# Kernel optimization log

Hardware: AMD Instinct MI355X
Metric: run time of the kernel (lower is better)

The kernel has to match this reference:

```python
import jax, jax.numpy as jnp
import numpy as np

TOKEN_DIM = 1024
N_HEADS = 16
HEAD_DIM = TOKEN_DIM // N_HEADS  # 64
B, S = 8, 1024


def setup_inputs() -> dict:
    key = jax.random.key(0)
    ks = jax.random.split(key, 7)
    scale = 1.0 / np.sqrt(HEAD_DIM)
    token_seq = jax.random.normal(ks[0], (B, S, TOKEN_DIM), dtype=jnp.float32)
    Wq = jax.random.normal(ks[1], (N_HEADS, HEAD_DIM, HEAD_DIM), dtype=jnp.float32) * scale
    Wk = jax.random.normal(ks[2], (N_HEADS, HEAD_DIM, HEAD_DIM), dtype=jnp.float32) * scale
    Wv = jax.random.normal(ks[3], (N_HEADS, HEAD_DIM, HEAD_DIM), dtype=jnp.float32) * scale
    bq = jax.random.normal(ks[4], (N_HEADS, HEAD_DIM), dtype=jnp.float32) * 0.01
    bk = jax.random.normal(ks[5], (N_HEADS, HEAD_DIM), dtype=jnp.float32) * 0.01
    bv = jax.random.normal(ks[6], (N_HEADS, HEAD_DIM), dtype=jnp.float32) * 0.01
    return {"token_seq": token_seq, "Wq": Wq, "Wk": Wk, "Wv": Wv,
            "bq": bq, "bk": bk, "bv": bv}


def reference(token_seq, Wq, Wk, Wv, bq, bk, bv):
    b, s, d = token_seq.shape
    x = token_seq.reshape(b, s, N_HEADS, HEAD_DIM)  # [B,S,H,hd]
    # Per-head linear projections (torch nn.Linear per head, batched as einsum)
    q = jnp.einsum('bshd,hde->bshe', x, Wq) + bq  # [B,S,H,hd]
    k = jnp.einsum('bshd,hde->bshe', x, Wk) + bk
    v = jnp.einsum('bshd,hde->bshe', x, Wv) + bv
    inv_sqrt_d = jnp.asarray(1.0 / np.sqrt(HEAD_DIM), dtype=token_seq.dtype)
    scores = jnp.einsum('bshe,bthe->bhst', q, k) * inv_sqrt_d  # [B,H,S,S]
    attn = jax.nn.softmax(scores, axis=-1)
    out = jnp.einsum('bhst,bthe->bshe', attn, v)  # [B,S,H,hd]
    # concat over heads along last dim == reshape
    return out.reshape(b, s, d)
```

## Files before the change

kernel.cpp:

```cpp
#include <hip/hip_runtime.h>
#include <stdint.h>

#define NH 16
#define HD 64
#define BB 8
#define SS 1024
#define TD 1024

typedef _Float16 f16;
typedef __attribute__((ext_vector_type(8))) f16 f16x8;
typedef __attribute__((ext_vector_type(16))) float f32x16;

#define MFMA32(a, b, c) __builtin_amdgcn_mfma_f32_32x32x16_f16((a), (b), (c), 0, 0, 0)
#define SW(r, c) (((r) << 7) + ((c) ^ (((r) & 7) << 4)))

__device__ __forceinline__ unsigned pkrtz(float a, float b) {
    auto r = __builtin_amdgcn_cvt_pkrtz(a, b);
    return __builtin_bit_cast(unsigned, r);
}
__device__ __forceinline__ unsigned h16(float a) {
    f16 h = (f16)a;
    return (unsigned)__builtin_bit_cast(unsigned short, h);
}
__device__ __forceinline__ unsigned pk_rtne(float a, float b) {
    return h16(a) | (h16(b) << 16);
}
__device__ __forceinline__ void gload16(const void* g, void* l) {
    __builtin_amdgcn_global_load_lds(
        (const __attribute__((address_space(1))) unsigned int*)g,
        (__attribute__((address_space(3))) unsigned int*)l, 16, 0, 0);
}

__global__ __launch_bounds__(256) void proj_kernel(
    const float* __restrict__ x,
    const float* __restrict__ Wq, const float* __restrict__ Wk, const float* __restrict__ Wv,
    const float* __restrict__ bq, const float* __restrict__ bk, const float* __restrict__ bv,
    f16* __restrict__ qo, f16* __restrict__ ko, f16* __restrict__ vo)
{
    __shared__ __align__(16) char lds[40960];
    const int stile = blockIdx.x, h = blockIdx.y, b = blockIdx.z;
    const int t = threadIdx.x;
    const int s0 = stile * 128;
    const int pair = b * NH + h;

    {
        const int row = t >> 1, half = t & 1;
        const float* src = x + ((size_t)b * SS + s0 + row) * TD + h * HD + half * 32;
        #pragma unroll
        for (int i = 0; i < 8; ++i) {
            float4 v4 = *(const float4*)(src + i * 4);
            const int cb = half * 64 + i * 8;
            *(unsigned*)(lds + SW(row, cb))     = pk_rtne(v4.x, v4.y);
            *(unsigned*)(lds + SW(row, cb + 4)) = pk_rtne(v4.z, v4.w);
        }
    }
    {
        const int e = t & 63, dg = t >> 6;
        const float* Ws[3] = {Wq, Wk, Wv};
        #pragma unroll
        for (int z = 0; z < 3; ++z) {
            const float* src = Ws[z] + (size_t)h * 4096 + (size_t)dg * 16 * 64 + e;
            char* base = lds + 16384 + z * 8192;
            #pragma unroll
            for (int j = 0; j < 8; ++j) {
                const float a0 = src[(2 * j) * 64], a1 = src[(2 * j + 1) * 64];
                const int cb = dg * 32 + j * 4;
                *(unsigned*)(base + SW(e, cb)) = pk_rtne(a0, a1);
            }
        }
    }
    __syncthreads();

    const int w = t >> 6, l = t & 63, l31 = l & 31, hi = l >> 5;
    const float* bs[3] = {bq, bk, bv};

    f16x8 xa[4];
    #pragma unroll
    for (int c = 0; c < 4; ++c)
        xa[c] = *(const f16x8*)(lds + SW(w * 32 + l31, c * 32 + hi * 16));

    #pragma unroll
    for (int z = 0; z < 2; ++z) {
        const char* wb = lds + 16384 + z * 8192;
        f32x16 acc[2] = {};
        #pragma unroll
        for (int nt = 0; nt < 2; ++nt)
            #pragma unroll
            for (int c = 0; c < 4; ++c) {
                f16x8 wf = *(const f16x8*)(wb + SW(nt * 32 + l31, c * 32 + hi * 16));
                acc[nt] = MFMA32(xa[c], wf, acc[nt]);
            }
        const float scl = (z == 0) ? 0.125f * 1.44269504088896f : 1.0f;
        f16* dst = (z == 0) ? qo : ko;
        #pragma unroll
        for (int nt = 0; nt < 2; ++nt) {
            const int e = nt * 32 + l31;
            const float bb = bs[z][h * 64 + e];
            #pragma unroll
            for (int r = 0; r < 16; ++r) {
                const int sl = w * 32 + (r & 3) + 8 * (r >> 2) + 4 * hi;
                dst[(size_t)pair * 65536 + (size_t)(s0 + sl) * 64 + e] =
                    (f16)((acc[nt][r] + bb) * scl);
            }
        }
    }
    {
        const char* wb = lds + 16384 + 2 * 8192;
        const int mt = w & 1, ng = w >> 1;
        f16x8 wv[4];
        #pragma unroll
        for (int c = 0; c < 4; ++c)
            wv[c] = *(const f16x8*)(wb + SW(mt * 32 + l31, c * 32 + hi * 16));
        float bvv[16];
        #pragma unroll
        for (int r = 0; r < 16; ++r)
            bvv[r] = bs[2][h * 64 + mt * 32 + (r & 3) + 8 * (r >> 2) + 4 * hi];
        f32x16 acc[2] = {};
        #pragma unroll
        for (int j = 0; j < 2; ++j) {
            const int srow = (ng * 2 + j) * 32 + l31;
            #pragma unroll
            for (int c = 0; c < 4; ++c) {
                f16x8 xf = *(const f16x8*)(lds + SW(srow, c * 32 + hi * 16));
                acc[j] = MFMA32(wv[c], xf, acc[j]);
            }
        }
        #pragma unroll
        for (int j = 0; j < 2; ++j) {
            const int sl = (ng * 2 + j) * 32 + l31;
            #pragma unroll
            for (int r = 0; r < 16; ++r) {
                const int e = mt * 32 + (r & 3) + 8 * (r >> 2) + 4 * hi;
                vo[(size_t)pair * 65536 + (size_t)e * 1024 + s0 + sl] =
                    (f16)(acc[j][r] + bvv[r]);
            }
        }
    }
}

__global__ __launch_bounds__(256, 4) void attn_kernel(
    const f16* __restrict__ qf, const f16* __restrict__ kf,
    const f16* __restrict__ vt, float* __restrict__ out)
{
    __shared__ __align__(16) char lds[32768];

    const int p = blockIdx.x;
    const int id = (p & 7) * 128 + (p >> 3);
    const int st = id & 7;
    const int pr = id >> 3;
    const int h = pr & (NH - 1), b = pr >> 4;

    const int t = threadIdx.x, w = t >> 6, l = t & 63, l31 = l & 31, hi = l >> 5;

    f16x8 qfr[4];
    {
        const char* qp = (const char*)(qf + (size_t)pr * 65536)
                       + (size_t)(st * 128 + w * 32 + l31) * 128;
        #pragma unroll
        for (int c = 0; c < 4; ++c)
            qfr[c] = *(const f16x8*)(qp + c * 32 + hi * 16);
    }

    int koff[2], voff[2];
    #pragma unroll
    for (int j = 0; j < 2; ++j) {
        const int o = j * 4096 + w * 1024 + l * 16;
        const int r = o >> 7, c = o & 127;
        const int cs = c ^ ((r & 7) << 4);
        koff[j] = r * 128 + cs;
        voff[j] = r * 2048 + cs;
    }
    const char* kB = (const char*)(kf + (size_t)pr * 65536);
    const char* vB = (const char*)(vt + (size_t)pr * 65536);

    auto stage = [&](int kt, int base) {
        #pragma unroll
        for (int j = 0; j < 2; ++j) {
            char* ld = lds + base + j * 4096 + w * 1024;
            gload16(kB + (size_t)kt * 8192 + koff[j], ld);
            gload16(vB + (size_t)kt * 128 + voff[j], ld + 8192);
        }
    };

    float m = -3e38f, lsum = 0.f;
    f32x16 o_[2] = {};

    stage(0, 0);

    for (int kt = 0; kt < 16; ++kt) {
        __syncthreads();
        const int X = (kt & 1) ? 16384 : 0;
        if (kt < 15) stage(kt + 1, 16384 - X);

        f32x16 s_[2] = {};
        #pragma unroll
        for (int jt = 0; jt < 2; ++jt)
            #pragma unroll
            for (int c = 0; c < 4; ++c) {
                f16x8 kfr = *(const f16x8*)(lds + X + SW(jt * 32 + l31, c * 32 + hi * 16));
                s_[jt] = MFMA32(kfr, qfr[c], s_[jt]);
            }

        float mm = s_[0][0];
        #pragma unroll
        for (int i = 1; i < 16; ++i) mm = fmaxf(mm, s_[0][i]);
        #pragma unroll
        for (int i = 0; i < 16; ++i) mm = fmaxf(mm, s_[1][i]);
        mm = fmaxf(mm, __shfl_xor(mm, 32));
        const float nm = fmaxf(m, mm);
        const float sc = __builtin_amdgcn_exp2f(m - nm);
        m = nm;
        float ps = 0.f;
        #pragma unroll
        for (int jt = 0; jt < 2; ++jt)
            #pragma unroll
            for (int i = 0; i < 16; ++i) {
                const float e = __builtin_amdgcn_exp2f(s_[jt][i] - nm);
                s_[jt][i] = e;
                ps += e;
            }
        ps += __shfl_xor(ps, 32);
        lsum = lsum * sc + ps;
        #pragma unroll
        for (int i = 0; i < 16; ++i) { o_[0][i] *= sc; o_[1][i] *= sc; }

        #pragma unroll
        for (int jt = 0; jt < 2; ++jt) {
            unsigned u[8];
            #pragma unroll
            for (int a = 0; a < 4; ++a) {
                u[2 * a]     = pkrtz(s_[jt][4 * a],     s_[jt][4 * a + 1]);
                u[2 * a + 1] = pkrtz(s_[jt][4 * a + 2], s_[jt][4 * a + 3]);
            }
            {
                auto r0 = __builtin_amdgcn_permlane32_swap(u[0], u[2], false, false);
                u[0] = r0[0]; u[2] = r0[1];
                auto r1 = __builtin_amdgcn_permlane32_swap(u[1], u[3], false, false);
                u[1] = r1[0]; u[3] = r1[1];
                auto r2 = __builtin_amdgcn_permlane32_swap(u[4], u[6], false, false);
                u[4] = r2[0]; u[6] = r2[1];
                auto r3 = __builtin_amdgcn_permlane32_swap(u[5], u[7], false, false);
                u[5] = r3[0]; u[7] = r3[1];
            }
            #pragma unroll
            for (int cl = 0; cl < 2; ++cl) {
                uint4 pu = {u[cl * 4], u[cl * 4 + 1], u[cl * 4 + 2], u[cl * 4 + 3]};
                f16x8 pf = __builtin_bit_cast(f16x8, pu);
                const int cv = jt * 2 + cl;
                #pragma unroll
                for (int mt = 0; mt < 2; ++mt) {
                    f16x8 vf = *(const f16x8*)(lds + X + 8192 + SW(mt * 32 + l31, cv * 32 + hi * 16));
                    o_[mt] = MFMA32(vf, pf, o_[mt]);
                }
            }
        }
    }

    const float inv = 1.0f / lsum;
    const size_t row = (size_t)b * SS + st * 128 + w * 32 + l31;
    float* op = out + row * TD + h * 64;
    #pragma unroll
    for (int mt = 0; mt < 2; ++mt)
        #pragma unroll
        for (int g = 0; g < 4; ++g) {
            const int e0 = mt * 32 + 8 * g + 4 * hi;
            float4 o4 = {o_[mt][4 * g] * inv, o_[mt][4 * g + 1] * inv,
                         o_[mt][4 * g + 2] * inv, o_[mt][4 * g + 3] * inv};
            *(float4*)(op + e0) = o4;
        }
}

extern "C" void kernel_launch(void* const* d_in, const int* in_sizes, int n_in,
                              void* d_out, int out_size, void* d_ws, size_t ws_size,
                              hipStream_t stream) {
    const float* x  = (const float*)d_in[0];
    const float* Wq = (const float*)d_in[1];
    const float* Wk = (const float*)d_in[2];
    const float* Wv = (const float*)d_in[3];
    const float* bq = (const float*)d_in[4];
    const float* bk = (const float*)d_in[5];
    const float* bv = (const float*)d_in[6];
    float* outp = (float*)d_out;

    const size_t per = (size_t)BB * NH * SS * HD;
    f16* q  = (f16*)d_ws;
    f16* k  = q + per;
    f16* vt = k + per;

    proj_kernel<<<dim3(SS / 128, NH, BB), dim3(256), 0, stream>>>(
        x, Wq, Wk, Wv, bq, bk, bv, q, k, vt);
    attn_kernel<<<dim3(1024), dim3(256), 0, stream>>>(q, k, vt, outp);
}
```

Before: 147.9 us.

## Add lazy softmax rescaling, packed f16 row sums, and vectorized projection stores

In the attention kernel, the running max and the rescale of the accumulators are updated only when some lane's tile max exceeds the current max by more than 8 (in log2 units). This skips most per-tile exp and multiply work on the output accumulators. Row sums are now computed from the packed f16 probabilities with half-precision vector adds, the max uses a tree reduction, LDS addresses are precomputed, and the loop is unrolled by two. The projection kernel swaps MFMA operand order so each lane owns contiguous outputs, which allows packed 8-byte stores instead of scalar f16 stores. The risks are f16 rounding in the sums and a larger dynamic range in the unnormalized exponentials.

```diff
diff --git a/kernel.cpp b/kernel.cpp
--- a/kernel.cpp
+++ b/kernel.cpp
@@ -8,6 +8,7 @@
 #define TD 1024
 
 typedef _Float16 f16;
+typedef __attribute__((ext_vector_type(2))) f16 h2;
 typedef __attribute__((ext_vector_type(8))) f16 f16x8;
 typedef __attribute__((ext_vector_type(16))) float f32x16;
 
@@ -18,6 +19,7 @@
     auto r = __builtin_amdgcn_cvt_pkrtz(a, b);
     return __builtin_bit_cast(unsigned, r);
 }
+__device__ __forceinline__ h2 B2(unsigned u) { return __builtin_bit_cast(h2, u); }
 __device__ __forceinline__ unsigned h16(float a) {
     f16 h = (f16)a;
     return (unsigned)__builtin_bit_cast(unsigned short, h);
@@ -88,21 +90,24 @@
             #pragma unroll
             for (int c = 0; c < 4; ++c) {
                 f16x8 wf = *(const f16x8*)(wb + SW(nt * 32 + l31, c * 32 + hi * 16));
-                acc[nt] = MFMA32(xa[c], wf, acc[nt]);
+                acc[nt] = MFMA32(wf, xa[c], acc[nt]);
             }
         const float scl = (z == 0) ? 0.125f * 1.44269504088896f : 1.0f;
-        f16* dst = (z == 0) ? qo : ko;
-        #pragma unroll
-        for (int nt = 0; nt < 2; ++nt) {
-            const int e = nt * 32 + l31;
-            const float bb = bs[z][h * 64 + e];
-            #pragma unroll
-            for (int r = 0; r < 16; ++r) {
-                const int sl = w * 32 + (r & 3) + 8 * (r >> 2) + 4 * hi;
-                dst[(size_t)pair * 65536 + (size_t)(s0 + sl) * 64 + e] =
-                    (f16)((acc[nt][r] + bb) * scl);
-            }
-        }
+        f16* row_ptr = ((z == 0) ? qo : ko)
+                     + (size_t)pair * 65536 + (size_t)(s0 + w * 32 + l31) * 64;
+        #pragma unroll
+        for (int nt = 0; nt < 2; ++nt)
+            #pragma unroll
+            for (int g = 0; g < 4; ++g) {
+                const int e0 = nt * 32 + 8 * g + 4 * hi;
+                const float4 bb = *(const float4*)(bs[z] + h * 64 + e0);
+                const float v0 = (acc[nt][4 * g + 0] + bb.x) * scl;
+                const float v1 = (acc[nt][4 * g + 1] + bb.y) * scl;
+                const float v2 = (acc[nt][4 * g + 2] + bb.z) * scl;
+                const float v3 = (acc[nt][4 * g + 3] + bb.w) * scl;
+                uint2 pv = {pk_rtne(v0, v1), pk_rtne(v2, v3)};
+                *(uint2*)(row_ptr + e0) = pv;
+            }
     }
     {
         const char* wb = lds + 16384 + 2 * 8192;
@@ -111,28 +116,26 @@
         #pragma unroll
         for (int c = 0; c < 4; ++c)
             wv[c] = *(const f16x8*)(wb + SW(mt * 32 + l31, c * 32 + hi * 16));
-        float bvv[16];
-        #pragma unroll
-        for (int r = 0; r < 16; ++r)
-            bvv[r] = bs[2][h * 64 + mt * 32 + (r & 3) + 8 * (r >> 2) + 4 * hi];
-        f32x16 acc[2] = {};
+        const float bvv = bs[2][h * 64 + mt * 32 + l31];
+        f16* vrow = vo + (size_t)pair * 65536 + (size_t)(mt * 32 + l31) * 1024 + s0;
         #pragma unroll
         for (int j = 0; j < 2; ++j) {
-            const int srow = (ng * 2 + j) * 32 + l31;
+            const int srow = (ng * 2 + j) * 32;
+            f32x16 acc = {};
             #pragma unroll
             for (int c = 0; c < 4; ++c) {
-                f16x8 xf = *(const f16x8*)(lds + SW(srow, c * 32 + hi * 16));
-                acc[j] = MFMA32(wv[c], xf, acc[j]);
-            }
-        }
-        #pragma unroll
-        for (int j = 0; j < 2; ++j) {
-            const int sl = (ng * 2 + j) * 32 + l31;
-            #pragma unroll
-            for (int r = 0; r < 16; ++r) {
-                const int e = mt * 32 + (r & 3) + 8 * (r >> 2) + 4 * hi;
-                vo[(size_t)pair * 65536 + (size_t)e * 1024 + s0 + sl] =
-                    (f16)(acc[j][r] + bvv[r]);
+                f16x8 xf = *(const f16x8*)(lds + SW(srow + l31, c * 32 + hi * 16));
+                acc = MFMA32(xf, wv[c], acc);
+            }
+            #pragma unroll
+            for (int g = 0; g < 4; ++g) {
+                const int sb = srow + 8 * g + 4 * hi;
+                const float v0 = acc[4 * g + 0] + bvv;
+                const float v1 = acc[4 * g + 1] + bvv;
+                const float v2 = acc[4 * g + 2] + bvv;
+                const float v3 = acc[4 * g + 3] + bvv;
+                uint2 pv = {pk_rtne(v0, v1), pk_rtne(v2, v3)};
+                *(uint2*)(vrow + sb) = pv;
             }
         }
     }
@@ -160,6 +163,11 @@
         for (int c = 0; c < 4; ++c)
             qfr[c] = *(const f16x8*)(qp + c * 32 + hi * 16);
     }
+
+    int adr[4];
+    #pragma unroll
+    for (int c = 0; c < 4; ++c)
+        adr[c] = (l31 << 7) + ((c * 32 + hi * 16) ^ ((l31 & 7) << 4));
 
     int koff[2], voff[2];
     #pragma unroll
@@ -187,69 +195,86 @@
 
     stage(0, 0);
 
+    #pragma unroll 2
     for (int kt = 0; kt < 16; ++kt) {
         __syncthreads();
-        const int X = (kt & 1) ? 16384 : 0;
-        if (kt < 15) stage(kt + 1, 16384 - X);
+        const int X = (kt & 1) << 14;
+        if (kt < 15) stage(kt + 1, X ^ 16384);
 
         f32x16 s_[2] = {};
         #pragma unroll
         for (int jt = 0; jt < 2; ++jt)
             #pragma unroll
             for (int c = 0; c < 4; ++c) {
-                f16x8 kfr = *(const f16x8*)(lds + X + SW(jt * 32 + l31, c * 32 + hi * 16));
+                f16x8 kfr = *(const f16x8*)(lds + X + jt * 4096 + adr[c]);
                 s_[jt] = MFMA32(kfr, qfr[c], s_[jt]);
             }
 
-        float mm = s_[0][0];
-        #pragma unroll
-        for (int i = 1; i < 16; ++i) mm = fmaxf(mm, s_[0][i]);
-        #pragma unroll
-        for (int i = 0; i < 16; ++i) mm = fmaxf(mm, s_[1][i]);
-        mm = fmaxf(mm, __shfl_xor(mm, 32));
-        const float nm = fmaxf(m, mm);
-        const float sc = __builtin_amdgcn_exp2f(m - nm);
-        m = nm;
-        float ps = 0.f;
+        float red[16];
+        #pragma unroll
+        for (int i = 0; i < 16; ++i) red[i] = fmaxf(s_[0][i], s_[1][i]);
+        #pragma unroll
+        for (int off = 8; off >= 1; off >>= 1)
+            #pragma unroll
+            for (int i = 0; i < off; ++i) red[i] = fmaxf(red[i], red[i + off]);
+        float mx = fmaxf(red[0], __shfl_xor(red[0], 32));
+
+        if (__any(mx > m + 8.0f)) {
+            const float nm = fmaxf(m, mx);
+            const float sc = __builtin_amdgcn_exp2f(m - nm);
+            m = nm;
+            lsum *= sc;
+            #pragma unroll
+            for (int i = 0; i < 16; ++i) { o_[0][i] *= sc; o_[1][i] *= sc; }
+        }
+
         #pragma unroll
         for (int jt = 0; jt < 2; ++jt)
             #pragma unroll
-            for (int i = 0; i < 16; ++i) {
-                const float e = __builtin_amdgcn_exp2f(s_[jt][i] - nm);
-                s_[jt][i] = e;
-                ps += e;
-            }
-        ps += __shfl_xor(ps, 32);
-        lsum = lsum * sc + ps;
-        #pragma unroll
-        for (int i = 0; i < 16; ++i) { o_[0][i] *= sc; o_[1][i] *= sc; }
+            for (int i = 0; i < 16; ++i)
+                s_[jt][i] = __builtin_amdgcn_exp2f(s_[jt][i] - m);
+
+        unsigned u[2][8];
+        #pragma unroll
+        for (int jt = 0; jt < 2; ++jt)
+            #pragma unroll
+            for (int a = 0; a < 4; ++a) {
+                u[jt][2 * a]     = pkrtz(s_[jt][4 * a],     s_[jt][4 * a + 1]);
+                u[jt][2 * a + 1] = pkrtz(s_[jt][4 * a + 2], s_[jt][4 * a + 3]);
+            }
+
+        {
+            h2 t0 = (B2(u[0][0]) + B2(u[0][1])) + (B2(u[0][2]) + B2(u[0][3]));
+            h2 t1 = (B2(u[0][4]) + B2(u[0][5])) + (B2(u[0][6]) + B2(u[0][7]));
+            h2 t2 = (B2(u[1][0]) + B2(u[1][1])) + (B2(u[1][2]) + B2(u[1][3]));
+            h2 t3 = (B2(u[1][4]) + B2(u[1][5])) + (B2(u[1][6]) + B2(u[1][7]));
+            h2 tt = (t0 + t1) + (t2 + t3);
+            float ps = (float)tt[0] + (float)tt[1];
+            ps += __shfl_xor(ps, 32);
+            lsum += ps;
+        }
 
         #pragma unroll
         for (int jt = 0; jt < 2; ++jt) {
-            unsigned u[8];
-            #pragma unroll
-            for (int a = 0; a < 4; ++a) {
-                u[2 * a]     = pkrtz(s_[jt][4 * a],     s_[jt][4 * a + 1]);
-                u[2 * a + 1] = pkrtz(s_[jt][4 * a + 2], s_[jt][4 * a + 3]);
-            }
+            unsigned* uj = u[jt];
             {
-                auto r0 = __builtin_amdgcn_permlane32_swap(u[0], u[2], false, false);
-                u[0] = r0[0]; u[2] = r0[1];
-                auto r1 = __builtin_amdgcn_permlane32_swap(u[1], u[3], false, false);
-                u[1] = r1[0]; u[3] = r1[1];
-                auto r2 = __builtin_amdgcn_permlane32_swap(u[4], u[6], false, false);
-                u[4] = r2[0]; u[6] = r2[1];
-                auto r3 = __builtin_amdgcn_permlane32_swap(u[5], u[7], false, false);
-                u[5] = r3[0]; u[7] = r3[1];
+                auto r0 = __builtin_amdgcn_permlane32_swap(uj[0], uj[2], false, false);
+                uj[0] = r0[0]; uj[2] = r0[1];
+                auto r1 = __builtin_amdgcn_permlane32_swap(uj[1], uj[3], false, false);
+                uj[1] = r1[0]; uj[3] = r1[1];
+                auto r2 = __builtin_amdgcn_permlane32_swap(uj[4], uj[6], false, false);
+                uj[4] = r2[0]; uj[6] = r2[1];
+                auto r3 = __builtin_amdgcn_permlane32_swap(uj[5], uj[7], false, false);
+                uj[5] = r3[0]; uj[7] = r3[1];
             }
             #pragma unroll
             for (int cl = 0; cl < 2; ++cl) {
-                uint4 pu = {u[cl * 4], u[cl * 4 + 1], u[cl * 4 + 2], u[cl * 4 + 3]};
+                uint4 pu = {uj[cl * 4], uj[cl * 4 + 1], uj[cl * 4 + 2], uj[cl * 4 + 3]};
                 f16x8 pf = __builtin_bit_cast(f16x8, pu);
                 const int cv = jt * 2 + cl;
                 #pragma unroll
                 for (int mt = 0; mt < 2; ++mt) {
-                    f16x8 vf = *(const f16x8*)(lds + X + 8192 + SW(mt * 32 + l31, cv * 32 + hi * 16));
+                    f16x8 vf = *(const f16x8*)(lds + X + 8192 + mt * 4096 + adr[cv]);
                     o_[mt] = MFMA32(vf, pf, o_[mt]);
                 }
             }
```

Measured after the change: 159.2 us. 1.08x slower.
